# Kernel optimization log

Measured on AMD Instinct MI355X. Metric: run time of the kernel, lower is better.

The kernel has to match this reference:

```python
import jax, jax.numpy as jnp
import numpy as np

NUM_USERS = 200000
NUM_ITEMS = 100000
N_NODES = NUM_USERS + NUM_ITEMS
NNZ = 4000000
LATENT_DIM = 64
N_LAYERS = 3


def setup_inputs() -> dict:
    key = jax.random.key(0)
    k1, k2, k3, k4, k5 = jax.random.split(key, 5)
    user_emb = jax.random.normal(k1, (NUM_USERS, LATENT_DIM), dtype=jnp.float32) * 0.1
    item_emb = jax.random.normal(k2, (NUM_ITEMS, LATENT_DIM), dtype=jnp.float32) * 0.1
    vals = jax.random.uniform(k3, (NNZ,), dtype=jnp.float32)
    rows = jax.random.randint(k4, (NNZ,), 0, N_NODES)
    cols = jax.random.randint(k5, (NNZ,), 0, N_NODES)
    return {"user_emb": user_emb, "item_emb": item_emb, "vals": vals,
            "rows": rows, "cols": cols}


def _spmm(vals, rows, cols, x):
    # y[r] += vals[e] * x[cols[e]]  -- COO SpMM, equivalent to torch.sparse.mm
    msgs = vals[:, None] * x[cols]          # [nnz, d]
    return jax.ops.segment_sum(msgs, rows, num_segments=N_NODES)


def reference(user_emb, item_emb, vals, rows, cols):
    # LightGCN.computer(), eval path: L = ones, no dropout, norm_emb=False
    all_emb = jnp.concatenate([user_emb, item_emb], axis=0)  # [N, d]
    emb = all_emb
    acc = all_emb
    for _ in range(N_LAYERS):
        emb = _spmm(vals, rows, cols, emb)
        acc = acc + emb
    light_out = acc / jnp.asarray(N_LAYERS + 1, dtype=acc.dtype)  # mean over layers
    users = light_out[:NUM_USERS]
    items = light_out[NUM_USERS:]
    return users, items
```

## Files before the change

### kernel.cpp

```cpp
#include <hip/hip_runtime.h>

#define NUM_USERS 200000
#define NUM_ITEMS 100000
#define N_NODES   300000
#define NNZ       4000000
#define DIM       64
#define N_ELEM   ((size_t)N_NODES * DIM)

#define BKT_SHIFT 8
#define BKT_ROWS  256
#define NBKT      ((N_NODES + BKT_ROWS - 1) >> BKT_SHIFT)
#define NSUB      8
#define PAD       32

typedef unsigned int uint32;

static __device__ __forceinline__ unsigned short f2bf(float f) {
    unsigned int u = __float_as_uint(f);
    u = (u + 0x7FFF + ((u >> 16) & 1)) >> 16;
    return (unsigned short)u;
}

__global__ void lgcn_convert(const float4* __restrict__ user4,
                             const float4* __restrict__ item4,
                             ushort4* __restrict__ bufC) {
    size_t i = (size_t)blockIdx.x * blockDim.x + threadIdx.x;
    const size_t n4 = N_ELEM / 4, nu4 = (size_t)NUM_USERS * DIM / 4;
    if (i >= n4) return;
    float4 v = (i < nu4) ? user4[i] : item4[i - nu4];
    ushort4 o;
    o.x = f2bf(v.x); o.y = f2bf(v.y); o.z = f2bf(v.z); o.w = f2bf(v.w);
    bufC[i] = o;
}

__global__ void lgcn_bhist(const int4* __restrict__ rows4, int* __restrict__ bcnt) {
    int i = blockIdx.x * blockDim.x + threadIdx.x;
    if (i >= NNZ / 4) return;
    int g = (i >> 6) & (NSUB - 1);
    int4 r = rows4[i];
    atomicAdd(&bcnt[(((r.x >> BKT_SHIFT) << 3) + g) * PAD], 1);
    atomicAdd(&bcnt[(((r.y >> BKT_SHIFT) << 3) + g) * PAD], 1);
    atomicAdd(&bcnt[(((r.z >> BKT_SHIFT) << 3) + g) * PAD], 1);
    atomicAdd(&bcnt[(((r.w >> BKT_SHIFT) << 3) + g) * PAD], 1);
}

__global__ void lgcn_balloc(const int* __restrict__ bcnt, int* __restrict__ bbase,
                            int* __restrict__ btot, int* __restrict__ bfill,
                            int* __restrict__ cursor) {
    int b = blockIdx.x * blockDim.x + threadIdx.x;
    int lane = threadIdx.x & 63;
    int cg[NSUB];
    int tot = 0;
    if (b < NBKT) {
        #pragma unroll
        for (int g = 0; g < NSUB; ++g) {
            cg[g] = bcnt[((b << 3) + g) * PAD];
            tot += cg[g];
        }
    }
    int s = tot;
    #pragma unroll
    for (int o = 1; o < 64; o <<= 1) {
        int t = __shfl_up(s, o);
        if (lane >= o) s += t;
    }
    int wtot = __shfl(s, 63);
    int wbase = 0;
    if (lane == 63) wbase = atomicAdd(cursor, wtot);
    wbase = __shfl(wbase, 63);
    if (b < NBKT) {
        int base = wbase + (s - tot);
        bbase[b] = base;
        btot[b]  = tot;
        int run = base;
        #pragma unroll
        for (int g = 0; g < NSUB; ++g) {
            bfill[((b << 3) + g) * PAD] = run;
            run += cg[g];
        }
    }
}

__global__ void lgcn_append(const int* __restrict__ rows, const int* __restrict__ cols,
                            const float* __restrict__ vals, int* __restrict__ bfill,
                            int2* __restrict__ staging) {
    int e = blockIdx.x * blockDim.x + threadIdx.x;
    if (e >= NNZ) return;
    int g = blockIdx.x & (NSUB - 1);
    int r = rows[e];
    int b = r >> BKT_SHIFT;
    int p = atomicAdd(&bfill[((b << 3) + g) * PAD], 1);
    staging[p] = make_int2(((r & (BKT_ROWS - 1)) << 19) | cols[e],
                           __float_as_int(vals[e]));
}

__global__ __launch_bounds__(256) void lgcn_bsort(
    const int2* __restrict__ staging, const int* __restrict__ bbase,
    const int* __restrict__ btot, int2* __restrict__ desc, int2* __restrict__ sc)
{
    __shared__ int cnt[BKT_ROWS], pfx[BKT_ROWS], fill[BKT_ROWS];
    int b   = blockIdx.x;
    int tid = threadIdx.x;
    cnt[tid] = 0;
    __syncthreads();
    int base = bbase[b];
    int n    = btot[b];

    for (int i = tid; i < n; i += 256)
        atomicAdd(&cnt[staging[base + i].x >> 19], 1);
    __syncthreads();

    int c = cnt[tid];
    pfx[tid] = c;
    __syncthreads();
    for (int o = 1; o < 256; o <<= 1) {
        int t = (tid >= o) ? pfx[tid - o] : 0;
        __syncthreads();
        pfx[tid] += t;
        __syncthreads();
    }
    int excl = pfx[tid] - c;
    fill[tid] = excl;
    int row = (b << BKT_SHIFT) + tid;
    if (row < N_NODES) desc[row] = make_int2(base + excl, c);
    __syncthreads();

    for (int i = tid; i < n; i += 256) {
        int2 e = staging[base + i];
        int lr = e.x >> 19;
        int p = atomicAdd(&fill[lr], 1);
        sc[base + p] = make_int2(e.x & 0x7FFFF, e.y);
    }
}

template<int MODE>
__global__ __launch_bounds__(256) void lgcn_spmm_csr(
    const int2* __restrict__ desc, const int2* __restrict__ sc,
    const uint32* __restrict__ cur2, uint32* __restrict__ nxt2,
    const float2* __restrict__ user2, const float2* __restrict__ item2,
    const uint32* __restrict__ e1b, const uint32* __restrict__ e2b,
    float2* __restrict__ out2)
{
    int row  = blockIdx.x * 4 + (threadIdx.x >> 6);
    int lane = threadIdx.x & 63;
    if (row >= N_NODES) return;
    int2 d = desc[row];
    int b = d.x, n = d.y;
    int half = lane >> 5;
    int hl   = lane & 31;
    float accA_lo = 0.f, accA_hi = 0.f, accB_lo = 0.f, accB_hi = 0.f;

    for (int k0 = 0; k0 < n; k0 += 64) {
        int m = min(64, n - k0);
        int c = 0, vbits = 0;
        if (lane < m) {
            int2 cv = sc[b + k0 + lane];
            c = cv.x; vbits = cv.y;
        }
        int m16 = (m + 15) & ~15;
        for (int j = 0; j < m16; j += 16) {
            int    idx[8];
            float  vv[8];
            uint32 x[8];
            #pragma unroll
            for (int t = 0; t < 8; ++t) {
                int src = j + 2 * t + half;
                idx[t] = __shfl(c, src);
                vv[t]  = __int_as_float(__shfl(vbits, src));
            }
            #pragma unroll
            for (int t = 0; t < 8; ++t)
                x[t] = cur2[idx[t] * 32 + hl];
            #pragma unroll
            for (int t = 0; t < 8; ++t) {
                float xlo = __uint_as_float(x[t] << 16);
                float xhi = __uint_as_float(x[t] & 0xFFFF0000u);
                if (t & 1) { accB_lo += vv[t] * xlo; accB_hi += vv[t] * xhi; }
                else       { accA_lo += vv[t] * xlo; accA_hi += vv[t] * xhi; }
            }
        }
    }

    float alo = accA_lo + accB_lo;
    float ahi = accA_hi + accB_hi;
    alo += __shfl_xor(alo, 32);
    ahi += __shfl_xor(ahi, 32);

    if (half == 0) {
        int off = row * 32 + hl;
        if constexpr (MODE == 1) {
            nxt2[off] = ((uint32)f2bf(ahi) << 16) | (uint32)f2bf(alo);
        } else {
            float2 own = (row < NUM_USERS) ? user2[off]
                                           : item2[(row - NUM_USERS) * 32 + hl];
            uint32 e1 = e1b[off], e2 = e2b[off];
            float2 o;
            o.x = 0.25f * (own.x + __uint_as_float(e1 << 16)
                                 + __uint_as_float(e2 << 16) + alo);
            o.y = 0.25f * (own.y + __uint_as_float(e1 & 0xFFFF0000u)
                                 + __uint_as_float(e2 & 0xFFFF0000u) + ahi);
            out2[off] = o;
        }
    }
}

extern "C" void kernel_launch(void* const* d_in, const int* in_sizes, int n_in,
                              void* d_out, int out_size, void* d_ws, size_t ws_size,
                              hipStream_t stream) {
    const float* user_emb = (const float*)d_in[0];
    const float* item_emb = (const float*)d_in[1];
    const float* vals     = (const float*)d_in[2];
    const int*   rows     = (const int*)d_in[3];
    const int*   cols     = (const int*)d_in[4];
    float* out = (float*)d_out;

    char* ws = (char*)d_ws;
    size_t off = 0;
    unsigned short* bufC = (unsigned short*)(ws + off); off += N_ELEM * 2;
    unsigned short* buf0 = (unsigned short*)(ws + off); off += N_ELEM * 2;
    unsigned short* buf1 = (unsigned short*)(ws + off); off += N_ELEM * 2;
    int2* staging = (int2*)(ws + off); off += (size_t)NNZ * 8;
    int2* sc      = (int2*)(ws + off); off += (size_t)NNZ * 8;
    int2* desc    = (int2*)(ws + off); off += (size_t)N_NODES * 8;
    int*  bcnt    = (int*) (ws + off); off += (size_t)NBKT * NSUB * PAD * 4;
    int*  cursor  = (int*) (ws + off); off += 256;
    int*  bbase   = (int*) (ws + off); off += (size_t)NBKT * 4;
    int*  btot    = (int*) (ws + off); off += (size_t)NBKT * 4;
    int*  bfill   = (int*) (ws + off); off += (size_t)NBKT * NSUB * PAD * 4;

    const int BLK = 256;
    dim3 grid_conv((unsigned)((N_ELEM / 4 + BLK - 1) / BLK));
    dim3 grid_edge((NNZ + BLK - 1) / BLK);
    dim3 grid_edge4((NNZ / 4 + BLK - 1) / BLK);
    dim3 grid_bkt((NBKT + BLK - 1) / BLK);
    dim3 grid_sort(NBKT);
    dim3 grid_spmm((N_NODES + 3) / 4);

    hipMemsetAsync(bcnt, 0, (size_t)NBKT * NSUB * PAD * 4 + 256, stream);
    lgcn_convert<<<grid_conv, BLK, 0, stream>>>(
        (const float4*)user_emb, (const float4*)item_emb, (ushort4*)bufC);
    lgcn_bhist<<<grid_edge4, BLK, 0, stream>>>((const int4*)rows, bcnt);
    lgcn_balloc<<<grid_bkt, BLK, 0, stream>>>(bcnt, bbase, btot, bfill, cursor);
    lgcn_append<<<grid_edge, BLK, 0, stream>>>(rows, cols, vals, bfill, staging);
    lgcn_bsort<<<grid_sort, BLK, 0, stream>>>(staging, bbase, btot, desc, sc);

    lgcn_spmm_csr<1><<<grid_spmm, BLK, 0, stream>>>(
        desc, sc, (const uint32*)bufC, (uint32*)buf0,
        nullptr, nullptr, nullptr, nullptr, nullptr);
    lgcn_spmm_csr<1><<<grid_spmm, BLK, 0, stream>>>(
        desc, sc, (const uint32*)buf0, (uint32*)buf1,
        nullptr, nullptr, nullptr, nullptr, nullptr);
    lgcn_spmm_csr<2><<<grid_spmm, BLK, 0, stream>>>(
        desc, sc, (const uint32*)buf1, nullptr,
        (const float2*)user_emb, (const float2*)item_emb,
        (const uint32*)buf0, (const uint32*)buf1, (float2*)out);
}
```

Measured before the change: 857.7 us.

## Replace bucketed two-pass sort with direct per-row counting sort for CSR build

Builds the CSR directly with per-row histograms split into 8 sub-counters, a wave-level scan that writes row descriptors, and a single scatter of (col,val) pairs to final positions. This removes the staging buffer, the bucket allocation and the shared-memory per-bucket sort kernel. In exchange it uses many more scattered global atomics on a larger counter array. The within-row edge order is now nondeterministic.

```diff
diff --git a/kernel.cpp b/kernel.cpp
--- a/kernel.cpp
+++ b/kernel.cpp
@@ -7,11 +7,8 @@
 #define DIM       64
 #define N_ELEM   ((size_t)N_NODES * DIM)
 
-#define BKT_SHIFT 8
-#define BKT_ROWS  256
-#define NBKT      ((N_NODES + BKT_ROWS - 1) >> BKT_SHIFT)
 #define NSUB      8
-#define PAD       32
+#define NROWBLK   ((N_NODES + 255) / 256)
 
 typedef unsigned int uint32;
 
@@ -33,28 +30,28 @@
     bufC[i] = o;
 }
 
-__global__ void lgcn_bhist(const int4* __restrict__ rows4, int* __restrict__ bcnt) {
+__global__ void lgcn_rhist(const int4* __restrict__ rows4, int* __restrict__ cnt) {
     int i = blockIdx.x * blockDim.x + threadIdx.x;
     if (i >= NNZ / 4) return;
-    int g = (i >> 6) & (NSUB - 1);
+    int g = (i >> 8) & (NSUB - 1);
+    int* c = cnt + g * N_NODES;
     int4 r = rows4[i];
-    atomicAdd(&bcnt[(((r.x >> BKT_SHIFT) << 3) + g) * PAD], 1);
-    atomicAdd(&bcnt[(((r.y >> BKT_SHIFT) << 3) + g) * PAD], 1);
-    atomicAdd(&bcnt[(((r.z >> BKT_SHIFT) << 3) + g) * PAD], 1);
-    atomicAdd(&bcnt[(((r.w >> BKT_SHIFT) << 3) + g) * PAD], 1);
-}
-
-__global__ void lgcn_balloc(const int* __restrict__ bcnt, int* __restrict__ bbase,
-                            int* __restrict__ btot, int* __restrict__ bfill,
-                            int* __restrict__ cursor) {
-    int b = blockIdx.x * blockDim.x + threadIdx.x;
+    atomicAdd(&c[r.x], 1);
+    atomicAdd(&c[r.y], 1);
+    atomicAdd(&c[r.z], 1);
+    atomicAdd(&c[r.w], 1);
+}
+
+__global__ void lgcn_rscan(const int* __restrict__ cnt, int2* __restrict__ desc,
+                           int* __restrict__ fill, int* __restrict__ cursor) {
+    int row  = blockIdx.x * blockDim.x + threadIdx.x;
     int lane = threadIdx.x & 63;
     int cg[NSUB];
     int tot = 0;
-    if (b < NBKT) {
+    if (row < N_NODES) {
         #pragma unroll
         for (int g = 0; g < NSUB; ++g) {
-            cg[g] = bcnt[((b << 3) + g) * PAD];
+            cg[g] = cnt[g * N_NODES + row];
             tot += cg[g];
         }
     }
@@ -68,69 +65,37 @@
     int wbase = 0;
     if (lane == 63) wbase = atomicAdd(cursor, wtot);
     wbase = __shfl(wbase, 63);
-    if (b < NBKT) {
+    if (row < N_NODES) {
         int base = wbase + (s - tot);
-        bbase[b] = base;
-        btot[b]  = tot;
+        desc[row] = make_int2(base, tot);
         int run = base;
         #pragma unroll
         for (int g = 0; g < NSUB; ++g) {
-            bfill[((b << 3) + g) * PAD] = run;
+            fill[g * N_NODES + row] = run;
             run += cg[g];
         }
     }
 }
 
-__global__ void lgcn_append(const int* __restrict__ rows, const int* __restrict__ cols,
-                            const float* __restrict__ vals, int* __restrict__ bfill,
-                            int2* __restrict__ staging) {
-    int e = blockIdx.x * blockDim.x + threadIdx.x;
-    if (e >= NNZ) return;
-    int g = blockIdx.x & (NSUB - 1);
-    int r = rows[e];
-    int b = r >> BKT_SHIFT;
-    int p = atomicAdd(&bfill[((b << 3) + g) * PAD], 1);
-    staging[p] = make_int2(((r & (BKT_ROWS - 1)) << 19) | cols[e],
-                           __float_as_int(vals[e]));
-}
-
-__global__ __launch_bounds__(256) void lgcn_bsort(
-    const int2* __restrict__ staging, const int* __restrict__ bbase,
-    const int* __restrict__ btot, int2* __restrict__ desc, int2* __restrict__ sc)
-{
-    __shared__ int cnt[BKT_ROWS], pfx[BKT_ROWS], fill[BKT_ROWS];
-    int b   = blockIdx.x;
-    int tid = threadIdx.x;
-    cnt[tid] = 0;
-    __syncthreads();
-    int base = bbase[b];
-    int n    = btot[b];
-
-    for (int i = tid; i < n; i += 256)
-        atomicAdd(&cnt[staging[base + i].x >> 19], 1);
-    __syncthreads();
-
-    int c = cnt[tid];
-    pfx[tid] = c;
-    __syncthreads();
-    for (int o = 1; o < 256; o <<= 1) {
-        int t = (tid >= o) ? pfx[tid - o] : 0;
-        __syncthreads();
-        pfx[tid] += t;
-        __syncthreads();
-    }
-    int excl = pfx[tid] - c;
-    fill[tid] = excl;
-    int row = (b << BKT_SHIFT) + tid;
-    if (row < N_NODES) desc[row] = make_int2(base + excl, c);
-    __syncthreads();
-
-    for (int i = tid; i < n; i += 256) {
-        int2 e = staging[base + i];
-        int lr = e.x >> 19;
-        int p = atomicAdd(&fill[lr], 1);
-        sc[base + p] = make_int2(e.x & 0x7FFFF, e.y);
-    }
+__global__ void lgcn_scatter(const int4* __restrict__ rows4,
+                             const int4* __restrict__ cols4,
+                             const float4* __restrict__ vals4,
+                             int* __restrict__ fill, int2* __restrict__ sc) {
+    int i = blockIdx.x * blockDim.x + threadIdx.x;
+    if (i >= NNZ / 4) return;
+    int g = (i >> 8) & (NSUB - 1);
+    int* f = fill + g * N_NODES;
+    int4   r = rows4[i];
+    int4   c = cols4[i];
+    float4 v = vals4[i];
+    int p0 = atomicAdd(&f[r.x], 1);
+    int p1 = atomicAdd(&f[r.y], 1);
+    int p2 = atomicAdd(&f[r.z], 1);
+    int p3 = atomicAdd(&f[r.w], 1);
+    sc[p0] = make_int2(c.x, __float_as_int(v.x));
+    sc[p1] = make_int2(c.y, __float_as_int(v.y));
+    sc[p2] = make_int2(c.z, __float_as_int(v.z));
+    sc[p3] = make_int2(c.w, __float_as_int(v.w));
 }
 
 template<int MODE>
@@ -219,30 +184,25 @@
     unsigned short* bufC = (unsigned short*)(ws + off); off += N_ELEM * 2;
     unsigned short* buf0 = (unsigned short*)(ws + off); off += N_ELEM * 2;
     unsigned short* buf1 = (unsigned short*)(ws + off); off += N_ELEM * 2;
-    int2* staging = (int2*)(ws + off); off += (size_t)NNZ * 8;
     int2* sc      = (int2*)(ws + off); off += (size_t)NNZ * 8;
     int2* desc    = (int2*)(ws + off); off += (size_t)N_NODES * 8;
-    int*  bcnt    = (int*) (ws + off); off += (size_t)NBKT * NSUB * PAD * 4;
+    int*  cnt     = (int*) (ws + off); off += (size_t)NSUB * N_NODES * 4;
     int*  cursor  = (int*) (ws + off); off += 256;
-    int*  bbase   = (int*) (ws + off); off += (size_t)NBKT * 4;
-    int*  btot    = (int*) (ws + off); off += (size_t)NBKT * 4;
-    int*  bfill   = (int*) (ws + off); off += (size_t)NBKT * NSUB * PAD * 4;
+    int*  fill    = (int*) (ws + off); off += (size_t)NSUB * N_NODES * 4;
 
     const int BLK = 256;
     dim3 grid_conv((unsigned)((N_ELEM / 4 + BLK - 1) / BLK));
-    dim3 grid_edge((NNZ + BLK - 1) / BLK);
-    dim3 grid_edge4((NNZ / 4 + BLK - 1) / BLK);
-    dim3 grid_bkt((NBKT + BLK - 1) / BLK);
-    dim3 grid_sort(NBKT);
+    dim3 grid_e4((NNZ / 4 + BLK - 1) / BLK);
+    dim3 grid_scan(NROWBLK);
     dim3 grid_spmm((N_NODES + 3) / 4);
 
-    hipMemsetAsync(bcnt, 0, (size_t)NBKT * NSUB * PAD * 4 + 256, stream);
+    hipMemsetAsync(cnt, 0, (size_t)NSUB * N_NODES * 4 + 256, stream);
     lgcn_convert<<<grid_conv, BLK, 0, stream>>>(
         (const float4*)user_emb, (const float4*)item_emb, (ushort4*)bufC);
-    lgcn_bhist<<<grid_edge4, BLK, 0, stream>>>((const int4*)rows, bcnt);
-    lgcn_balloc<<<grid_bkt, BLK, 0, stream>>>(bcnt, bbase, btot, bfill, cursor);
-    lgcn_append<<<grid_edge, BLK, 0, stream>>>(rows, cols, vals, bfill, staging);
-    lgcn_bsort<<<grid_sort, BLK, 0, stream>>>(staging, bbase, btot, desc, sc);
+    lgcn_rhist<<<grid_e4, BLK, 0, stream>>>((const int4*)rows, cnt);
+    lgcn_rscan<<<grid_scan, BLK, 0, stream>>>(cnt, desc, fill, cursor);
+    lgcn_scatter<<<grid_e4, BLK, 0, stream>>>(
+        (const int4*)rows, (const int4*)cols, (const float4*)vals, fill, sc);
 
     lgcn_spmm_csr<1><<<grid_spmm, BLK, 0, stream>>>(
         desc, sc, (const uint32*)bufC, (uint32*)buf0,
```

Result: slower. 958.8 us (+11.8%).

## Gather bf16 rows with 16-byte loads, eight edges per wavefront in parallel

Applied to the files above, without the earlier changes.

Reworks the SpMM inner loop so each wavefront is split into eight groups of eight lanes. Each lane loads a uint4 (8 bf16 values), so one wavefront gathers eight neighbor rows per load instead of two. This cuts the number of load instructions and shuffles per edge and raises memory-level parallelism. In exchange it needs a cross-group shuffle reduction and more accumulator registers, and each 128-byte row is fetched by only eight lanes.

```diff
diff --git a/kernel.cpp b/kernel.cpp
--- a/kernel.cpp
+++ b/kernel.cpp
@@ -20,6 +20,8 @@
     u = (u + 0x7FFF + ((u >> 16) & 1)) >> 16;
     return (unsigned short)u;
 }
+static __device__ __forceinline__ float blo(uint32 w) { return __uint_as_float(w << 16); }
+static __device__ __forceinline__ float bhi(uint32 w) { return __uint_as_float(w & 0xFFFF0000u); }
 
 __global__ void lgcn_convert(const float4* __restrict__ user4,
                              const float4* __restrict__ item4,
@@ -136,19 +138,20 @@
 template<int MODE>
 __global__ __launch_bounds__(256) void lgcn_spmm_csr(
     const int2* __restrict__ desc, const int2* __restrict__ sc,
-    const uint32* __restrict__ cur2, uint32* __restrict__ nxt2,
-    const float2* __restrict__ user2, const float2* __restrict__ item2,
-    const uint32* __restrict__ e1b, const uint32* __restrict__ e2b,
-    float2* __restrict__ out2)
+    const uint4* __restrict__ cur4, uint4* __restrict__ nxt4,
+    const float4* __restrict__ user4, const float4* __restrict__ item4,
+    const uint4* __restrict__ e1b4, const uint4* __restrict__ e2b4,
+    float4* __restrict__ out4)
 {
     int row  = blockIdx.x * 4 + (threadIdx.x >> 6);
     int lane = threadIdx.x & 63;
     if (row >= N_NODES) return;
     int2 d = desc[row];
     int b = d.x, n = d.y;
-    int half = lane >> 5;
-    int hl   = lane & 31;
-    float accA_lo = 0.f, accA_hi = 0.f, accB_lo = 0.f, accB_hi = 0.f;
+    int q  = lane >> 3;
+    int gl = lane & 7;
+    float aAlo[4] = {0.f, 0.f, 0.f, 0.f}, aAhi[4] = {0.f, 0.f, 0.f, 0.f};
+    float aBlo[4] = {0.f, 0.f, 0.f, 0.f}, aBhi[4] = {0.f, 0.f, 0.f, 0.f};
 
     for (int k0 = 0; k0 < n; k0 += 64) {
         int m = min(64, n - k0);
@@ -159,47 +162,63 @@
         }
         int m16 = (m + 15) & ~15;
         for (int j = 0; j < m16; j += 16) {
-            int    idx[8];
-            float  vv[8];
-            uint32 x[8];
-            #pragma unroll
-            for (int t = 0; t < 8; ++t) {
-                int src = j + 2 * t + half;
-                idx[t] = __shfl(c, src);
-                vv[t]  = __int_as_float(__shfl(vbits, src));
-            }
-            #pragma unroll
-            for (int t = 0; t < 8; ++t)
-                x[t] = cur2[idx[t] * 32 + hl];
-            #pragma unroll
-            for (int t = 0; t < 8; ++t) {
-                float xlo = __uint_as_float(x[t] << 16);
-                float xhi = __uint_as_float(x[t] & 0xFFFF0000u);
-                if (t & 1) { accB_lo += vv[t] * xlo; accB_hi += vv[t] * xhi; }
-                else       { accA_lo += vv[t] * xlo; accA_hi += vv[t] * xhi; }
-            }
-        }
-    }
-
-    float alo = accA_lo + accB_lo;
-    float ahi = accA_hi + accB_hi;
-    alo += __shfl_xor(alo, 32);
-    ahi += __shfl_xor(ahi, 32);
-
-    if (half == 0) {
-        int off = row * 32 + hl;
+            int   i0 = __shfl(c, j + q);
+            int   i1 = __shfl(c, j + 8 + q);
+            float v0 = __int_as_float(__shfl(vbits, j + q));
+            float v1 = __int_as_float(__shfl(vbits, j + 8 + q));
+            uint4 x0 = cur4[i0 * 8 + gl];
+            uint4 x1 = cur4[i1 * 8 + gl];
+            aAlo[0] += v0 * blo(x0.x); aAhi[0] += v0 * bhi(x0.x);
+            aAlo[1] += v0 * blo(x0.y); aAhi[1] += v0 * bhi(x0.y);
+            aAlo[2] += v0 * blo(x0.z); aAhi[2] += v0 * bhi(x0.z);
+            aAlo[3] += v0 * blo(x0.w); aAhi[3] += v0 * bhi(x0.w);
+            aBlo[0] += v1 * blo(x1.x); aBhi[0] += v1 * bhi(x1.x);
+            aBlo[1] += v1 * blo(x1.y); aBhi[1] += v1 * bhi(x1.y);
+            aBlo[2] += v1 * blo(x1.z); aBhi[2] += v1 * bhi(x1.z);
+            aBlo[3] += v1 * blo(x1.w); aBhi[3] += v1 * bhi(x1.w);
+        }
+    }
+
+    float rlo[4], rhi[4];
+    #pragma unroll
+    for (int p = 0; p < 4; ++p) {
+        rlo[p] = aAlo[p] + aBlo[p];
+        rhi[p] = aAhi[p] + aBhi[p];
+    }
+    #pragma unroll
+    for (int o = 8; o < 64; o <<= 1) {
+        #pragma unroll
+        for (int p = 0; p < 4; ++p) {
+            rlo[p] += __shfl_xor(rlo[p], o);
+            rhi[p] += __shfl_xor(rhi[p], o);
+        }
+    }
+
+    if (lane < 8) {
         if constexpr (MODE == 1) {
-            nxt2[off] = ((uint32)f2bf(ahi) << 16) | (uint32)f2bf(alo);
+            uint4 o;
+            o.x = ((uint32)f2bf(rhi[0]) << 16) | (uint32)f2bf(rlo[0]);
+            o.y = ((uint32)f2bf(rhi[1]) << 16) | (uint32)f2bf(rlo[1]);
+            o.z = ((uint32)f2bf(rhi[2]) << 16) | (uint32)f2bf(rlo[2]);
+            o.w = ((uint32)f2bf(rhi[3]) << 16) | (uint32)f2bf(rlo[3]);
+            nxt4[row * 8 + gl] = o;
         } else {
-            float2 own = (row < NUM_USERS) ? user2[off]
-                                           : item2[(row - NUM_USERS) * 32 + hl];
-            uint32 e1 = e1b[off], e2 = e2b[off];
-            float2 o;
-            o.x = 0.25f * (own.x + __uint_as_float(e1 << 16)
-                                 + __uint_as_float(e2 << 16) + alo);
-            o.y = 0.25f * (own.y + __uint_as_float(e1 & 0xFFFF0000u)
-                                 + __uint_as_float(e2 & 0xFFFF0000u) + ahi);
-            out2[off] = o;
+            const float4* own4 = (row < NUM_USERS)
+                ? user4 + (size_t)row * 16
+                : item4 + (size_t)(row - NUM_USERS) * 16;
+            float4 w0 = own4[gl * 2], w1 = own4[gl * 2 + 1];
+            uint4 e1 = e1b4[row * 8 + gl], e2 = e2b4[row * 8 + gl];
+            float4 o0, o1;
+            o0.x = 0.25f * (w0.x + blo(e1.x) + blo(e2.x) + rlo[0]);
+            o0.y = 0.25f * (w0.y + bhi(e1.x) + bhi(e2.x) + rhi[0]);
+            o0.z = 0.25f * (w0.z + blo(e1.y) + blo(e2.y) + rlo[1]);
+            o0.w = 0.25f * (w0.w + bhi(e1.y) + bhi(e2.y) + rhi[1]);
+            o1.x = 0.25f * (w1.x + blo(e1.z) + blo(e2.z) + rlo[2]);
+            o1.y = 0.25f * (w1.y + bhi(e1.z) + bhi(e2.z) + rhi[2]);
+            o1.z = 0.25f * (w1.z + blo(e1.w) + blo(e2.w) + rlo[3]);
+            o1.w = 0.25f * (w1.w + bhi(e1.w) + bhi(e2.w) + rhi[3]);
+            out4[(size_t)row * 16 + gl * 2]     = o0;
+            out4[(size_t)row * 16 + gl * 2 + 1] = o1;
         }
     }
 }
@@ -245,13 +264,13 @@
     lgcn_bsort<<<grid_sort, BLK, 0, stream>>>(staging, bbase, btot, desc, sc);
 
     lgcn_spmm_csr<1><<<grid_spmm, BLK, 0, stream>>>(
-        desc, sc, (const uint32*)bufC, (uint32*)buf0,
+        desc, sc, (const uint4*)bufC, (uint4*)buf0,
         nullptr, nullptr, nullptr, nullptr, nullptr);
     lgcn_spmm_csr<1><<<grid_spmm, BLK, 0, stream>>>(
-        desc, sc, (const uint32*)buf0, (uint32*)buf1,
+        desc, sc, (const uint4*)buf0, (uint4*)buf1,
         nullptr, nullptr, nullptr, nullptr, nullptr);
     lgcn_spmm_csr<2><<<grid_spmm, BLK, 0, stream>>>(
-        desc, sc, (const uint32*)buf1, nullptr,
-        (const float2*)user_emb, (const float2*)item_emb,
-        (const uint32*)buf0, (const uint32*)buf1, (float2*)out);
-}
+        desc, sc, (const uint4*)buf1, nullptr,
+        (const float4*)user_emb, (const float4*)item_emb,
+        (const uint4*)buf0, (const uint4*)buf1, (float4*)out);
+}
```

After: 897.9 us. 1.05x slower.

## Map four rows per wavefront with 8-byte gathers and nontemporal streaming loads

Applied to the files above, without the earlier changes.

The SpMM kernel now gives each 64-lane wavefront four rows, with 16 lanes per row, instead of one row split into two halves. Each lane gathers a uint2 (four bf16 values) per neighbor, which removes the cross-half reduction and reduces idle lanes on short rows, since rows average about 13 edges. Loop trip counts follow the longest row of the four, so lanes with shorter rows sit idle inside the wave. Streaming reads (the edge arrays, the fp32 inputs and the final-layer buffers) now use nontemporal loads to avoid polluting the cache that serves the embedding gathers.

```diff
diff --git a/kernel.cpp b/kernel.cpp
--- a/kernel.cpp
+++ b/kernel.cpp
@@ -15,11 +15,35 @@
 
 typedef unsigned int uint32;
 
+typedef __attribute__((ext_vector_type(4))) float         nfloat4;
+typedef __attribute__((ext_vector_type(4))) int           nint4;
+typedef __attribute__((ext_vector_type(2))) int           nint2;
+typedef __attribute__((ext_vector_type(2))) unsigned int  nuint2;
+
+static __device__ __forceinline__ float4 ntload(const float4* p) {
+    nfloat4 v = __builtin_nontemporal_load(reinterpret_cast<const nfloat4*>(p));
+    return make_float4(v.x, v.y, v.z, v.w);
+}
+static __device__ __forceinline__ int4 ntload(const int4* p) {
+    nint4 v = __builtin_nontemporal_load(reinterpret_cast<const nint4*>(p));
+    return make_int4(v.x, v.y, v.z, v.w);
+}
+static __device__ __forceinline__ int2 ntload(const int2* p) {
+    nint2 v = __builtin_nontemporal_load(reinterpret_cast<const nint2*>(p));
+    return make_int2(v.x, v.y);
+}
+static __device__ __forceinline__ uint2 ntload(const uint2* p) {
+    nuint2 v = __builtin_nontemporal_load(reinterpret_cast<const nuint2*>(p));
+    return make_uint2(v.x, v.y);
+}
+
 static __device__ __forceinline__ unsigned short f2bf(float f) {
     unsigned int u = __float_as_uint(f);
     u = (u + 0x7FFF + ((u >> 16) & 1)) >> 16;
     return (unsigned short)u;
 }
+static __device__ __forceinline__ float blo(uint32 w) { return __uint_as_float(w << 16); }
+static __device__ __forceinline__ float bhi(uint32 w) { return __uint_as_float(w & 0xFFFF0000u); }
 
 __global__ void lgcn_convert(const float4* __restrict__ user4,
                              const float4* __restrict__ item4,
@@ -27,7 +51,7 @@
     size_t i = (size_t)blockIdx.x * blockDim.x + threadIdx.x;
     const size_t n4 = N_ELEM / 4, nu4 = (size_t)NUM_USERS * DIM / 4;
     if (i >= n4) return;
-    float4 v = (i < nu4) ? user4[i] : item4[i - nu4];
+    float4 v = (i < nu4) ? ntload(&user4[i]) : ntload(&item4[i - nu4]);
     ushort4 o;
     o.x = f2bf(v.x); o.y = f2bf(v.y); o.z = f2bf(v.z); o.w = f2bf(v.w);
     bufC[i] = o;
@@ -37,7 +61,7 @@
     int i = blockIdx.x * blockDim.x + threadIdx.x;
     if (i >= NNZ / 4) return;
     int g = (i >> 6) & (NSUB - 1);
-    int4 r = rows4[i];
+    int4 r = ntload(&rows4[i]);
     atomicAdd(&bcnt[(((r.x >> BKT_SHIFT) << 3) + g) * PAD], 1);
     atomicAdd(&bcnt[(((r.y >> BKT_SHIFT) << 3) + g) * PAD], 1);
     atomicAdd(&bcnt[(((r.z >> BKT_SHIFT) << 3) + g) * PAD], 1);
@@ -87,11 +111,12 @@
     int e = blockIdx.x * blockDim.x + threadIdx.x;
     if (e >= NNZ) return;
     int g = blockIdx.x & (NSUB - 1);
-    int r = rows[e];
+    int r   = __builtin_nontemporal_load(&rows[e]);
+    int cl  = __builtin_nontemporal_load(&cols[e]);
+    float v = __builtin_nontemporal_load(&vals[e]);
     int b = r >> BKT_SHIFT;
     int p = atomicAdd(&bfill[((b << 3) + g) * PAD], 1);
-    staging[p] = make_int2(((r & (BKT_ROWS - 1)) << 19) | cols[e],
-                           __float_as_int(vals[e]));
+    staging[p] = make_int2(((r & (BKT_ROWS - 1)) << 19) | cl, __float_as_int(v));
 }
 
 __global__ __launch_bounds__(256) void lgcn_bsort(
@@ -136,71 +161,78 @@
 template<int MODE>
 __global__ __launch_bounds__(256) void lgcn_spmm_csr(
     const int2* __restrict__ desc, const int2* __restrict__ sc,
-    const uint32* __restrict__ cur2, uint32* __restrict__ nxt2,
-    const float2* __restrict__ user2, const float2* __restrict__ item2,
-    const uint32* __restrict__ e1b, const uint32* __restrict__ e2b,
-    float2* __restrict__ out2)
+    const uint2* __restrict__ cur2, uint2* __restrict__ nxt2,
+    const float4* __restrict__ user4, const float4* __restrict__ item4,
+    const uint2* __restrict__ e1b2, const uint2* __restrict__ e2b2,
+    float4* __restrict__ out4)
 {
-    int row  = blockIdx.x * 4 + (threadIdx.x >> 6);
     int lane = threadIdx.x & 63;
-    if (row >= N_NODES) return;
+    int grp  = lane >> 4;
+    int gl   = lane & 15;
+    int gb   = grp << 4;
+    int row  = blockIdx.x * 16 + (threadIdx.x >> 6) * 4 + grp;
     int2 d = desc[row];
     int b = d.x, n = d.y;
-    int half = lane >> 5;
-    int hl   = lane & 31;
-    float accA_lo = 0.f, accA_hi = 0.f, accB_lo = 0.f, accB_hi = 0.f;
-
-    for (int k0 = 0; k0 < n; k0 += 64) {
-        int m = min(64, n - k0);
+
+    int nmax = n;
+    nmax = max(nmax, __shfl_xor(nmax, 16));
+    nmax = max(nmax, __shfl_xor(nmax, 32));
+
+    float a0lo = 0.f, a0hi = 0.f, a1lo = 0.f, a1hi = 0.f;
+
+    for (int k0 = 0; k0 < nmax; k0 += 16) {
+        int m = n - k0;
         int c = 0, vbits = 0;
-        if (lane < m) {
-            int2 cv = sc[b + k0 + lane];
+        if (gl < m) {
+            int2 cv = ntload(&sc[b + k0 + gl]);
             c = cv.x; vbits = cv.y;
         }
-        int m16 = (m + 15) & ~15;
-        for (int j = 0; j < m16; j += 16) {
-            int    idx[8];
-            float  vv[8];
-            uint32 x[8];
-            #pragma unroll
-            for (int t = 0; t < 8; ++t) {
-                int src = j + 2 * t + half;
-                idx[t] = __shfl(c, src);
-                vv[t]  = __int_as_float(__shfl(vbits, src));
-            }
-            #pragma unroll
-            for (int t = 0; t < 8; ++t)
-                x[t] = cur2[idx[t] * 32 + hl];
-            #pragma unroll
-            for (int t = 0; t < 8; ++t) {
-                float xlo = __uint_as_float(x[t] << 16);
-                float xhi = __uint_as_float(x[t] & 0xFFFF0000u);
-                if (t & 1) { accB_lo += vv[t] * xlo; accB_hi += vv[t] * xhi; }
-                else       { accA_lo += vv[t] * xlo; accA_hi += vv[t] * xhi; }
-            }
-        }
-    }
-
-    float alo = accA_lo + accB_lo;
-    float ahi = accA_hi + accB_hi;
-    alo += __shfl_xor(alo, 32);
-    ahi += __shfl_xor(ahi, 32);
-
-    if (half == 0) {
-        int off = row * 32 + hl;
-        if constexpr (MODE == 1) {
-            nxt2[off] = ((uint32)f2bf(ahi) << 16) | (uint32)f2bf(alo);
-        } else {
-            float2 own = (row < NUM_USERS) ? user2[off]
-                                           : item2[(row - NUM_USERS) * 32 + hl];
-            uint32 e1 = e1b[off], e2 = e2b[off];
-            float2 o;
-            o.x = 0.25f * (own.x + __uint_as_float(e1 << 16)
-                                 + __uint_as_float(e2 << 16) + alo);
-            o.y = 0.25f * (own.y + __uint_as_float(e1 & 0xFFFF0000u)
-                                 + __uint_as_float(e2 & 0xFFFF0000u) + ahi);
-            out2[off] = o;
-        }
+        int mp = min(max(m, 0), 16);
+        mp = max(mp, __shfl_xor(mp, 16));
+        mp = max(mp, __shfl_xor(mp, 32));
+        mp = (mp + 3) & ~3;
+        for (int j = 0; j < mp; j += 4) {
+            int   i0 = __shfl(c, gb + j);
+            int   i1 = __shfl(c, gb + j + 1);
+            int   i2 = __shfl(c, gb + j + 2);
+            int   i3 = __shfl(c, gb + j + 3);
+            float v0 = __int_as_float(__shfl(vbits, gb + j));
+            float v1 = __int_as_float(__shfl(vbits, gb + j + 1));
+            float v2 = __int_as_float(__shfl(vbits, gb + j + 2));
+            float v3 = __int_as_float(__shfl(vbits, gb + j + 3));
+            uint2 x0 = cur2[(size_t)i0 * 16 + gl];
+            uint2 x1 = cur2[(size_t)i1 * 16 + gl];
+            uint2 x2 = cur2[(size_t)i2 * 16 + gl];
+            uint2 x3 = cur2[(size_t)i3 * 16 + gl];
+            a0lo += v0 * blo(x0.x); a0hi += v0 * bhi(x0.x);
+            a1lo += v0 * blo(x0.y); a1hi += v0 * bhi(x0.y);
+            a0lo += v1 * blo(x1.x); a0hi += v1 * bhi(x1.x);
+            a1lo += v1 * blo(x1.y); a1hi += v1 * bhi(x1.y);
+            a0lo += v2 * blo(x2.x); a0hi += v2 * bhi(x2.x);
+            a1lo += v2 * blo(x2.y); a1hi += v2 * bhi(x2.y);
+            a0lo += v3 * blo(x3.x); a0hi += v3 * bhi(x3.x);
+            a1lo += v3 * blo(x3.y); a1hi += v3 * bhi(x3.y);
+        }
+    }
+
+    if constexpr (MODE == 1) {
+        uint2 o;
+        o.x = ((uint32)f2bf(a0hi) << 16) | (uint32)f2bf(a0lo);
+        o.y = ((uint32)f2bf(a1hi) << 16) | (uint32)f2bf(a1lo);
+        nxt2[(size_t)row * 16 + gl] = o;
+    } else {
+        const float4* ownp = (row < NUM_USERS)
+            ? &user4[(size_t)row * 16 + gl]
+            : &item4[(size_t)(row - NUM_USERS) * 16 + gl];
+        float4 w = ntload(ownp);
+        uint2 e1 = ntload(&e1b2[(size_t)row * 16 + gl]);
+        uint2 e2 = ntload(&e2b2[(size_t)row * 16 + gl]);
+        float4 o;
+        o.x = 0.25f * (w.x + blo(e1.x) + blo(e2.x) + a0lo);
+        o.y = 0.25f * (w.y + bhi(e1.x) + bhi(e2.x) + a0hi);
+        o.z = 0.25f * (w.z + blo(e1.y) + blo(e2.y) + a1lo);
+        o.w = 0.25f * (w.w + bhi(e1.y) + bhi(e2.y) + a1hi);
+        out4[(size_t)row * 16 + gl] = o;
     }
 }
 
@@ -234,9 +266,9 @@
     dim3 grid_edge4((NNZ / 4 + BLK - 1) / BLK);
     dim3 grid_bkt((NBKT + BLK - 1) / BLK);
     dim3 grid_sort(NBKT);
-    dim3 grid_spmm((N_NODES + 3) / 4);
-
-    hipMemsetAsync(bcnt, 0, (size_t)NBKT * NSUB * PAD * 4 + 256, stream);
+    dim3 grid_spmm(N_NODES / 16);
+
+    (void)hipMemsetAsync(bcnt, 0, (size_t)NBKT * NSUB * PAD * 4 + 256, stream);
     lgcn_convert<<<grid_conv, BLK, 0, stream>>>(
         (const float4*)user_emb, (const float4*)item_emb, (ushort4*)bufC);
     lgcn_bhist<<<grid_edge4, BLK, 0, stream>>>((const int4*)rows, bcnt);
@@ -245,13 +277,13 @@
     lgcn_bsort<<<grid_sort, BLK, 0, stream>>>(staging, bbase, btot, desc, sc);
 
     lgcn_spmm_csr<1><<<grid_spmm, BLK, 0, stream>>>(
-        desc, sc, (const uint32*)bufC, (uint32*)buf0,
+        desc, sc, (const uint2*)bufC, (uint2*)buf0,
         nullptr, nullptr, nullptr, nullptr, nullptr);
     lgcn_spmm_csr<1><<<grid_spmm, BLK, 0, stream>>>(
-        desc, sc, (const uint32*)buf0, (uint32*)buf1,
+        desc, sc, (const uint2*)buf0, (uint2*)buf1,
         nullptr, nullptr, nullptr, nullptr, nullptr);
     lgcn_spmm_csr<2><<<grid_spmm, BLK, 0, stream>>>(
-        desc, sc, (const uint32*)buf1, nullptr,
-        (const float2*)user_emb, (const float2*)item_emb,
-        (const uint32*)buf0, (const uint32*)buf1, (float2*)out);
-}
+        desc, sc, (const uint2*)buf1, nullptr,
+        (const float4*)user_emb, (const float4*)item_emb,
+        (const uint2*)buf0, (const uint2*)buf1, (float4*)out);
+}
```

Measured after the change: 798.8 us. 1.07x faster.
